# Performance work log

Hardware: AMD Instinct MI355X
Metric: run time of the kernel (lower is better)

Reference implementation:

```python
import jax, jax.numpy as jnp
import numpy as np
import math

B, S, H, NH = 2, 2048, 2048, 16
HD = H // NH
LAYER_NUMBER = 5
NORM_FACTOR = math.sqrt(HD) * LAYER_NUMBER  # sqrt(head_dim) * coeff
BETA = 1.0 / LAYER_NUMBER
SCALE = float(LAYER_NUMBER)  # ScaledSoftmax scale = coeff
MASK_VALUE = -10000.0


def setup_inputs() -> dict:
    key = jax.random.key(0)
    ks = jax.random.split(key, 6)
    inv_sqrt_h = 1.0 / math.sqrt(H)
    return {
        "hidden_states": jax.random.normal(ks[0], (B, S, H), jnp.float32),
        "alibi": jax.random.normal(ks[1], (NH, 1, S), jnp.float32) * 0.1,
        "w_qkv": jax.random.normal(ks[2], (3 * H, H), jnp.float32) * inv_sqrt_h,
        "b_qkv": jax.random.normal(ks[3], (3 * H,), jnp.float32) * 0.02,
        "w_dense": jax.random.normal(ks[4], (H, H), jnp.float32) * inv_sqrt_h,
        "b_dense": jax.random.normal(ks[5], (H,), jnp.float32) * 0.02,
        "attention_mask": jnp.ones((B, S), jnp.int32),
    }


def reference(hidden_states, alibi, w_qkv, b_qkv, w_dense, b_dense, attention_mask):
    b, s, h = hidden_states.shape
    # QKV projection: [b, s, 3h] -> [b, s, nh, 3*hd] -> split
    mixed = hidden_states @ w_qkv.T + b_qkv
    mixed = mixed.reshape(b, s, NH, 3 * HD)
    q, k, v = jnp.split(mixed, 3, axis=-1)  # each [b, s, nh, hd]

    # Faithful Megatron-style memory reinterpretation (row-major reshape),
    # exactly matching torch's .contiguous().view(s, b*nh, hd).
    q2 = jnp.swapaxes(q.reshape(s, b * NH, HD), 0, 1)  # [b*nh, q_len, hd]
    k2 = jnp.swapaxes(k.reshape(s, b * NH, HD), 0, 1)  # [b*nh, k_len, hd]
    v2 = jnp.swapaxes(v.reshape(s, b * NH, HD), 0, 1)  # [b*nh, k_len, hd]

    # baddbmm: alibi*beta + (q @ k^T)/norm_factor
    alibi_b = jnp.tile(alibi, (b, 1, 1))[: b * NH, :, :s]  # [b*nh, 1, k_len]
    scores = alibi_b * BETA + jnp.einsum("bqd,bkd->bqk", q2, k2) * (1.0 / NORM_FACTOR)
    scores = scores.reshape(b, NH, s, s)

    # ScaledSoftmax: scale then fused causal+padding mask fill, then softmax
    scores = scores * SCALE
    pad_bool = (1 - attention_mask).astype(bool)  # True where padded
    causal = jnp.tril(jnp.ones((s, s), dtype=bool))
    bad = pad_bool[:, None, :, None] | (~causal)[None, None, :, :]  # [b,1,s,s]
    scores = jnp.where(bad, MASK_VALUE, scores)
    probs = jax.nn.softmax(scores, axis=-1)  # [b, nh, s, s]

    # context = probs @ V with the same faithful reshapes
    probs_r = probs.reshape(b * NH, s, s)
    context = jnp.einsum("bqk,bkd->bqd", probs_r, v2)  # [b*nh, q_len, hd]
    context = context.reshape(b, NH, s, HD)
    context = jnp.transpose(context, (2, 0, 1, 3)).reshape(s, b, h)  # [s, b, h]

    out = context @ w_dense.T + b_dense  # [s, b, h]
    return jnp.swapaxes(out, 0, 1)  # [b, s, h]
```

## Files before the change

kernel.cpp:

```cpp
#include <hip/hip_runtime.h>

typedef unsigned short u16;
typedef __bf16  bf16x8 __attribute__((ext_vector_type(8)));
typedef float   f32x4  __attribute__((ext_vector_type(4)));
typedef u16     u16x8  __attribute__((ext_vector_type(8)));
typedef u16     u16x4  __attribute__((ext_vector_type(4)));

#define QSCALE 0.12751744545f

__device__ __forceinline__ u16 f2b(float f) {
    unsigned u = __float_as_uint(f);
    unsigned r = u + 0x7FFFu + ((u >> 16) & 1u);
    return (u16)(r >> 16);
}
__device__ __forceinline__ float b2f(u16 b) {
    return __uint_as_float(((unsigned)b) << 16);
}
__device__ __forceinline__ void async16(const u16* g, u16* l) {
    __builtin_amdgcn_global_load_lds(
        (__attribute__((address_space(1))) void*)(u16*)g,
        (__attribute__((address_space(3))) void*)l, 16, 0, 0);
}

__global__ void cvt_f32_bf16(const float* __restrict__ in, u16* __restrict__ out, int n4) {
    int i = blockIdx.x * blockDim.x + threadIdx.x;
    if (i >= n4) return;
    float4 f = ((const float4*)in)[i];
    u16x4 o;
    o[0] = f2b(f.x); o[1] = f2b(f.y); o[2] = f2b(f.z); o[3] = f2b(f.w);
    *(u16x4*)(out + (size_t)i * 4) = o;
}

__global__ void cvt_wqkv(const float* __restrict__ in, u16* __restrict__ out, int n4) {
    int i = blockIdx.x * blockDim.x + threadIdx.x;
    if (i >= n4) return;
    int row = i >> 9;
    float s = ((row % 384) < 128) ? QSCALE : 1.0f;
    float4 f = ((const float4*)in)[i];
    u16x4 o;
    o[0] = f2b(f.x * s); o[1] = f2b(f.y * s); o[2] = f2b(f.z * s); o[3] = f2b(f.w * s);
    *(u16x4*)(out + (size_t)i * 4) = o;
}

__global__ __launch_bounds__(256) void gemm_bt(
    const u16* __restrict__ A, const u16* __restrict__ B,
    const float* __restrict__ bias, void* __restrict__ C,
    u16* __restrict__ qb, u16* __restrict__ kb, u16* __restrict__ vb,
    int M, int N, int K, int mode)
{
    __shared__ u16 smem[16384];
    u16* As = smem;
    u16* Bs = smem + 8192;

    int tid = threadIdx.x, wave = tid >> 6, lane = tid & 63;
    int lg = lane >> 4, lm = lane & 15;
    int wm = (wave & 1) * 64, wn = (wave >> 1) * 64;

    const u16* Ab = A + (size_t)(blockIdx.y * 128) * K;
    const u16* Bb = B + (size_t)(blockIdx.x * 128) * K;

    f32x4 acc[4][4];
    for (int i = 0; i < 4; i++)
        for (int j = 0; j < 4; j++)
            acc[i][j] = (f32x4){0.f, 0.f, 0.f, 0.f};

    int srow = (lane >> 2), skq = (lane & 3) * 8;

    for (int k0 = 0; k0 < K; k0 += 64) {
        __syncthreads();
        for (int cc = wave; cc < 16; cc += 4) {
            int p = cc >> 3, c = cc & 7;
            int row = c * 16 + srow;
            size_t off = (size_t)row * K + k0 + p * 32 + skq;
            async16(Ab + off, &As[p * 4096 + c * 512]);
            async16(Bb + off, &Bs[p * 4096 + c * 512]);
        }
        __syncthreads();

        for (int p = 0; p < 2; p++) {
            bf16x8 af[4], bf[4];
            for (int i = 0; i < 4; i++) af[i] = *(const bf16x8*)&As[p * 4096 + (wm + i * 16 + lm) * 32 + lg * 8];
            for (int j = 0; j < 4; j++) bf[j] = *(const bf16x8*)&Bs[p * 4096 + (wn + j * 16 + lm) * 32 + lg * 8];
            for (int i = 0; i < 4; i++)
                for (int j = 0; j < 4; j++)
                    acc[i][j] = __builtin_amdgcn_mfma_f32_16x16x32_bf16(af[i], bf[j], acc[i][j], 0, 0, 0);
        }
    }

    if (mode == 1) {
        for (int j = 0; j < 4; j++) {
            int col = blockIdx.x * 128 + wn + j * 16 + lm;
            float bv = bias[col];
            for (int i = 0; i < 4; i++) {
                int row0 = blockIdx.y * 128 + wm + i * 16 + lg * 4;
                for (int r = 0; r < 4; r++) {
                    int row = row0 + r;
                    int orow = ((row & 1) << 11) + (row >> 1);
                    ((float*)C)[(size_t)orow * N + col] = acc[i][j][r] + bv;
                }
            }
        }
        return;
    }

    int ct = blockIdx.x;
    int nh = ct / 3, part = ct - nh * 3;
    float bscale = (part == 0) ? QSCALE : 1.0f;
    int rbase = blockIdx.y * 128;
    int b = rbase >> 11;
    int s0 = rbase & 2047;

    if (part < 2) {
        u16* dst0 = part ? kb : qb;
        for (int j = 0; j < 4; j++) {
            int hd = wn + j * 16 + lm;
            float bv = bias[ct * 128 + hd] * bscale;
            for (int i = 0; i < 4; i++) {
                for (int r = 0; r < 4; r++) {
                    int rl = wm + i * 16 + lg * 4 + r;
                    int s = s0 + rl;
                    int bn = (s & 1) * 16 + nh;
                    int pos = (b << 10) + (s >> 1);
                    dst0[((size_t)(bn * 2048 + pos)) * 128 + hd] = f2b(acc[i][j][r] + bv);
                }
            }
        }
    } else {
        u16 (*arr)[64][128] = (u16(*)[64][128])smem;
        __syncthreads();
        for (int j = 0; j < 4; j++) {
            int hd = wn + j * 16 + lm;
            float bv = bias[ct * 128 + hd];
            for (int i = 0; i < 4; i++) {
                for (int r = 0; r < 4; r++) {
                    int rl = wm + i * 16 + lg * 4 + r;
                    arr[rl & 1][rl >> 1][hd] = f2b(acc[i][j][r] + bv);
                }
            }
        }
        __syncthreads();
        int hd = tid & 127, par = tid >> 7;
        int bn = par * 16 + nh;
        int pos0 = (b << 10) + (s0 >> 1);
        u16* dst = vb + ((size_t)(bn * 128 + hd)) * 2048 + pos0;
        for (int c = 0; c < 8; c++) {
            u16x8 w;
            for (int e = 0; e < 8; e++) w[e] = arr[par][c * 8 + e][hd];
            *(u16x8*)(dst + c * 8) = w;
        }
    }
}

__global__ __launch_bounds__(256) void attn(
    const u16* __restrict__ qb, const u16* __restrict__ kb,
    const u16* __restrict__ vb, const float* __restrict__ alibi,
    u16* __restrict__ ctx)
{
    __shared__ u16 Ks[64 * 136];
    __shared__ u16 Vt[128 * 88];
    __shared__ u16 Ps[4][16 * 72];

    int bn = blockIdx.y;
    int tid = threadIdx.x, wave = tid >> 6, lane = tid & 63;
    int lg = lane >> 4, lm = lane & 15;

    const float* al = alibi + (bn & 15) * 2048;

    int krow = tid >> 2, kq = (tid & 3) * 32;
    int vhd  = tid >> 1, vh2 = (tid & 1) * 32;
    const u16* ksrc0 = kb + (size_t)(bn * 2048 + krow) * 128 + kq;
    const u16* vsrc0 = vb + (size_t)(bn * 128 + vhd) * 2048 + vh2;

    u16* ps = &Ps[wave][0];
    bf16x8 ones;
    {
        u16x8 t;
        for (int j = 0; j < 8; j++) t[j] = 0x3F80;
        ones = *(bf16x8*)&t;
    }

    for (int pass = 0; pass < 2; pass++) {
        int qt = pass ? (31 - blockIdx.x) : blockIdx.x;
        int q0 = qt * 64;

        bf16x8 qf[4];
        {
            const u16* qp = qb + ((size_t)bn * 2048 + q0 + wave * 16 + lm) * 128 + lg * 8;
            for (int kc = 0; kc < 4; kc++) qf[kc] = *(const bf16x8*)(qp + kc * 32);
        }

        f32x4 o[9];
        for (int i = 0; i < 9; i++) o[i] = (f32x4){0.f, 0.f, 0.f, 0.f};

        u16x8 kreg[4], vreg[4];
        for (int i = 0; i < 4; i++) kreg[i] = *(const u16x8*)(ksrc0 + i * 8);
        for (int i = 0; i < 4; i++) vreg[i] = *(const u16x8*)(vsrc0 + i * 8);

        for (int kt = 0; kt <= qt; kt++) {
            int k0 = kt * 64;
            __syncthreads();
            {
                u16* d1 = &Ks[krow * 136 + kq];
                for (int i = 0; i < 4; i++) *(u16x8*)(d1 + i * 8) = kreg[i];
                u16* d2 = &Vt[vhd * 88 + vh2];
                for (int i = 0; i < 4; i++) *(u16x8*)(d2 + i * 8) = vreg[i];
            }
            __syncthreads();

            if (kt < qt) {
                const u16* s1 = ksrc0 + (size_t)(kt + 1) * 64 * 128;
                const u16* s2 = vsrc0 + (kt + 1) * 64;
                for (int i = 0; i < 4; i++) kreg[i] = *(const u16x8*)(s1 + i * 8);
                for (int i = 0; i < 4; i++) vreg[i] = *(const u16x8*)(s2 + i * 8);
            }

            f32x4 sc[4];
            for (int tc = 0; tc < 4; tc++) {
                const u16* kr = &Ks[(tc * 16 + lm) * 136 + lg * 8];
                f32x4 a = (f32x4){0.f, 0.f, 0.f, 0.f};
                for (int kc = 0; kc < 4; kc++)
                    a = __builtin_amdgcn_mfma_f32_16x16x32_bf16(qf[kc], *(const bf16x8*)(kr + kc * 32), a, 0, 0, 0);
                sc[tc] = a;
            }

            bool diag = (kt == qt);
            for (int tc = 0; tc < 4; tc++) {
                int kg = k0 + tc * 16 + lm;
                float av = (al[kg] - 8.0f) * 1.4426950408889634f;
                for (int r = 0; r < 4; r++) {
                    float v = sc[tc][r] + av;
                    if (diag && kg > q0 + wave * 16 + lg * 4 + r) v = -3e38f;
                    ps[(lg * 4 + r) * 72 + tc * 16 + lm] = f2b(__builtin_amdgcn_exp2f(v));
                }
            }

            for (int kc = 0; kc < 2; kc++) {
                bf16x8 pf = *(const bf16x8*)&ps[lm * 72 + kc * 32 + lg * 8];
                for (int i = 0; i < 8; i++) {
                    bf16x8 vf = *(const bf16x8*)&Vt[(i * 16 + lm) * 88 + kc * 32 + lg * 8];
                    o[i] = __builtin_amdgcn_mfma_f32_16x16x32_bf16(pf, vf, o[i], 0, 0, 0);
                }
                o[8] = __builtin_amdgcn_mfma_f32_16x16x32_bf16(pf, ones, o[8], 0, 0, 0);
            }
        }

        for (int r = 0; r < 4; r++) {
            float inv = 1.0f / o[8][r];
            int qg = q0 + wave * 16 + lg * 4 + r;
            int row = qg * 2 + (bn >> 4);
            u16* crow = ctx + (size_t)row * 2048 + (bn & 15) * 128 + lm;
            for (int i = 0; i < 8; i++)
                crow[i * 16] = f2b(o[i][r] * inv);
        }
    }
}

extern "C" void kernel_launch(void* const* d_in, const int* in_sizes, int n_in,
                              void* d_out, int out_size, void* d_ws, size_t ws_size,
                              hipStream_t stream)
{
    const float* hs    = (const float*)d_in[0];
    const float* alibi = (const float*)d_in[1];
    const float* wqkv  = (const float*)d_in[2];
    const float* bqkv  = (const float*)d_in[3];
    const float* wd    = (const float*)d_in[4];
    const float* bd    = (const float*)d_in[5];
    float* out = (float*)d_out;

    char* ws = (char*)d_ws;
    u16* wqkv_b = (u16*)(ws + 0);
    u16* hs_b   = (u16*)(ws + 25165824);
    u16* ctx    = (u16*)(ws + 41943040);
    u16* wd_b   = wqkv_b;
    u16* qb     = (u16*)(ws + 92274688);
    u16* kb     = (u16*)(ws + 109051904);
    u16* vb     = (u16*)(ws + 125829120);

    cvt_f32_bf16<<<8192,  256, 0, stream>>>(hs,   hs_b,   2097152);
    cvt_wqkv   <<<12288, 256, 0, stream>>>(wqkv, wqkv_b, 3145728);

    gemm_bt<<<dim3(48, 32), 256, 0, stream>>>(hs_b, wqkv_b, bqkv, nullptr,
                                              qb, kb, vb, 4096, 6144, 2048, 0);

    cvt_f32_bf16<<<4096, 256, 0, stream>>>(wd, wd_b, 1048576);

    attn<<<dim3(16, 32), 256, 0, stream>>>(qb, kb, vb, alibi, ctx);

    gemm_bt<<<dim3(16, 32), 256, 0, stream>>>(ctx, wd_b, bd, out,
                                              nullptr, nullptr, nullptr, 4096, 2048, 2048, 1);
}
```

Before: 399.2 us.

## Use 32x32 MFMA with 128-row query tiles and double-buffered K/V in attention

Result: slower. 500.0 us (+25.3%).

```diff
diff --git a/kernel.cpp b/kernel.cpp
--- a/kernel.cpp
+++ b/kernel.cpp
@@ -3,6 +3,7 @@
 typedef unsigned short u16;
 typedef __bf16  bf16x8 __attribute__((ext_vector_type(8)));
 typedef float   f32x4  __attribute__((ext_vector_type(4)));
+typedef float   f32x16 __attribute__((ext_vector_type(16)));
 typedef u16     u16x8  __attribute__((ext_vector_type(8)));
 typedef u16     u16x4  __attribute__((ext_vector_type(4)));
 
@@ -151,18 +152,18 @@
     }
 }
 
-__global__ __launch_bounds__(256) void attn(
+__global__ __launch_bounds__(256, 1) void attn(
     const u16* __restrict__ qb, const u16* __restrict__ kb,
     const u16* __restrict__ vb, const float* __restrict__ alibi,
     u16* __restrict__ ctx)
 {
-    __shared__ u16 Ks[64 * 136];
-    __shared__ u16 Vt[128 * 88];
-    __shared__ u16 Ps[4][16 * 72];
+    __shared__ u16 Ks[2][64 * 140];
+    __shared__ u16 Vt[2][128 * 90];
+    __shared__ u16 Ps[4][32 * 74];
 
     int bn = blockIdx.y;
     int tid = threadIdx.x, wave = tid >> 6, lane = tid & 63;
-    int lg = lane >> 4, lm = lane & 15;
+    int ln = lane & 31, lh = lane >> 5;
 
     const float* al = alibi + (bn & 15) * 2048;
 
@@ -180,77 +181,85 @@
     }
 
     for (int pass = 0; pass < 2; pass++) {
-        int qt = pass ? (31 - blockIdx.x) : blockIdx.x;
-        int q0 = qt * 64;
-
-        bf16x8 qf[4];
+        int qt = pass ? (15 - blockIdx.x) : blockIdx.x;
+        int q0w = qt * 128 + wave * 32;
+        int ktmax = 2 * qt + 1;
+
+        bf16x8 qf[8];
         {
-            const u16* qp = qb + ((size_t)bn * 2048 + q0 + wave * 16 + lm) * 128 + lg * 8;
-            for (int kc = 0; kc < 4; kc++) qf[kc] = *(const bf16x8*)(qp + kc * 32);
-        }
-
-        f32x4 o[9];
-        for (int i = 0; i < 9; i++) o[i] = (f32x4){0.f, 0.f, 0.f, 0.f};
+            const u16* qp = qb + ((size_t)bn * 2048 + q0w + ln) * 128 + lh * 8;
+            for (int ks = 0; ks < 8; ks++) qf[ks] = *(const bf16x8*)(qp + ks * 16);
+        }
+
+        f32x16 o[4], sums;
+        for (int e = 0; e < 16; e++) { sums[e] = 0.f; o[0][e] = 0.f; o[1][e] = 0.f; o[2][e] = 0.f; o[3][e] = 0.f; }
 
         u16x8 kreg[4], vreg[4];
         for (int i = 0; i < 4; i++) kreg[i] = *(const u16x8*)(ksrc0 + i * 8);
         for (int i = 0; i < 4; i++) vreg[i] = *(const u16x8*)(vsrc0 + i * 8);
-
-        for (int kt = 0; kt <= qt; kt++) {
+        {
+            u16* d1 = &Ks[0][krow * 140 + kq];
+            for (int i = 0; i < 4; i++) *(u16x8*)(d1 + i * 8) = kreg[i];
+            u16* d2 = &Vt[0][vhd * 90 + vh2];
+            for (int i = 0; i < 4; i++) *(u16x8*)(d2 + i * 8) = vreg[i];
+        }
+        __syncthreads();
+
+        for (int kt = 0; kt <= ktmax; kt++) {
+            int cur = kt & 1;
             int k0 = kt * 64;
-            __syncthreads();
-            {
-                u16* d1 = &Ks[krow * 136 + kq];
-                for (int i = 0; i < 4; i++) *(u16x8*)(d1 + i * 8) = kreg[i];
-                u16* d2 = &Vt[vhd * 88 + vh2];
-                for (int i = 0; i < 4; i++) *(u16x8*)(d2 + i * 8) = vreg[i];
-            }
-            __syncthreads();
-
-            if (kt < qt) {
+
+            if (kt < ktmax) {
                 const u16* s1 = ksrc0 + (size_t)(kt + 1) * 64 * 128;
                 const u16* s2 = vsrc0 + (kt + 1) * 64;
                 for (int i = 0; i < 4; i++) kreg[i] = *(const u16x8*)(s1 + i * 8);
                 for (int i = 0; i < 4; i++) vreg[i] = *(const u16x8*)(s2 + i * 8);
             }
 
-            f32x4 sc[4];
-            for (int tc = 0; tc < 4; tc++) {
-                const u16* kr = &Ks[(tc * 16 + lm) * 136 + lg * 8];
-                f32x4 a = (f32x4){0.f, 0.f, 0.f, 0.f};
-                for (int kc = 0; kc < 4; kc++)
-                    a = __builtin_amdgcn_mfma_f32_16x16x32_bf16(qf[kc], *(const bf16x8*)(kr + kc * 32), a, 0, 0, 0);
-                sc[tc] = a;
-            }
-
-            bool diag = (kt == qt);
-            for (int tc = 0; tc < 4; tc++) {
-                int kg = k0 + tc * 16 + lm;
+            bool domask = (k0 + 63 > q0w);
+            for (int ct = 0; ct < 2; ct++) {
+                const u16* kr = &Ks[cur][(ct * 32 + ln) * 140 + lh * 8];
+                f32x16 a;
+                for (int e = 0; e < 16; e++) a[e] = 0.f;
+                for (int ks = 0; ks < 8; ks++)
+                    a = __builtin_amdgcn_mfma_f32_32x32x16_bf16(qf[ks], *(const bf16x8*)(kr + ks * 16), a, 0, 0, 0);
+
+                int kg = k0 + ct * 32 + ln;
                 float av = (al[kg] - 8.0f) * 1.4426950408889634f;
-                for (int r = 0; r < 4; r++) {
-                    float v = sc[tc][r] + av;
-                    if (diag && kg > q0 + wave * 16 + lg * 4 + r) v = -3e38f;
-                    ps[(lg * 4 + r) * 72 + tc * 16 + lm] = f2b(__builtin_amdgcn_exp2f(v));
-                }
-            }
-
-            for (int kc = 0; kc < 2; kc++) {
-                bf16x8 pf = *(const bf16x8*)&ps[lm * 72 + kc * 32 + lg * 8];
-                for (int i = 0; i < 8; i++) {
-                    bf16x8 vf = *(const bf16x8*)&Vt[(i * 16 + lm) * 88 + kc * 32 + lg * 8];
-                    o[i] = __builtin_amdgcn_mfma_f32_16x16x32_bf16(pf, vf, o[i], 0, 0, 0);
-                }
-                o[8] = __builtin_amdgcn_mfma_f32_16x16x32_bf16(pf, ones, o[8], 0, 0, 0);
-            }
-        }
-
-        for (int r = 0; r < 4; r++) {
-            float inv = 1.0f / o[8][r];
-            int qg = q0 + wave * 16 + lg * 4 + r;
-            int row = qg * 2 + (bn >> 4);
-            u16* crow = ctx + (size_t)row * 2048 + (bn & 15) * 128 + lm;
-            for (int i = 0; i < 8; i++)
-                crow[i * 16] = f2b(o[i][r] * inv);
+                for (int reg = 0; reg < 16; reg++) {
+                    int row = (reg & 3) + 8 * (reg >> 2) + 4 * lh;
+                    float v = a[reg] + av;
+                    if (domask && kg > q0w + row) v = -3e38f;
+                    ps[row * 74 + ct * 32 + ln] = f2b(__builtin_amdgcn_exp2f(v));
+                }
+            }
+
+            for (int ks = 0; ks < 4; ks++) {
+                bf16x8 pa = *(const bf16x8*)&ps[ln * 74 + ks * 16 + lh * 8];
+                sums = __builtin_amdgcn_mfma_f32_32x32x16_bf16(pa, ones, sums, 0, 0, 0);
+                for (int ht = 0; ht < 4; ht++) {
+                    bf16x8 vf = *(const bf16x8*)&Vt[cur][(ht * 32 + ln) * 90 + ks * 16 + lh * 8];
+                    o[ht] = __builtin_amdgcn_mfma_f32_32x32x16_bf16(pa, vf, o[ht], 0, 0, 0);
+                }
+            }
+
+            if (kt < ktmax) {
+                u16* d1 = &Ks[cur ^ 1][krow * 140 + kq];
+                for (int i = 0; i < 4; i++) *(u16x8*)(d1 + i * 8) = kreg[i];
+                u16* d2 = &Vt[cur ^ 1][vhd * 90 + vh2];
+                for (int i = 0; i < 4; i++) *(u16x8*)(d2 + i * 8) = vreg[i];
+            }
+            __syncthreads();
+        }
+
+        for (int reg = 0; reg < 16; reg++) {
+            int row = (reg & 3) + 8 * (reg >> 2) + 4 * lh;
+            float inv = 1.0f / sums[reg];
+            int qg = q0w + row;
+            int crow = qg * 2 + (bn >> 4);
+            u16* cp = ctx + (size_t)crow * 2048 + (bn & 15) * 128 + ln;
+            for (int ht = 0; ht < 4; ht++)
+                cp[ht * 32] = f2b(o[ht][reg] * inv);
         }
     }
 }
@@ -284,7 +293,7 @@
 
     cvt_f32_bf16<<<4096, 256, 0, stream>>>(wd, wd_b, 1048576);
 
-    attn<<<dim3(16, 32), 256, 0, stream>>>(qb, kb, vb, alibi, ctx);
+    attn<<<dim3(8, 32), 256, 0, stream>>>(qb, kb, vb, alibi, ctx);
 
     gemm_bt<<<dim3(16, 32), 256, 0, stream>>>(ctx, wd_b, bd, out,
                                               nullptr, nullptr, nullptr, 4096, 2048, 2048, 1);
```

## Split causal attention KV range across two blocks with fp32 partials and finalize kernel

Applied to the files above, without the earlier changes.

Measured after the change: 463.8 us. 16.2% more time.

```diff
diff --git a/kernel.cpp b/kernel.cpp
--- a/kernel.cpp
+++ b/kernel.cpp
@@ -151,16 +151,16 @@
     }
 }
 
-__global__ __launch_bounds__(256) void attn(
+__global__ __launch_bounds__(256, 2) void attn(
     const u16* __restrict__ qb, const u16* __restrict__ kb,
     const u16* __restrict__ vb, const float* __restrict__ alibi,
-    u16* __restrict__ ctx)
+    float* __restrict__ Opart, float* __restrict__ Spart)
 {
-    __shared__ u16 Ks[64 * 136];
-    __shared__ u16 Vt[128 * 88];
-    __shared__ u16 Ps[4][16 * 72];
-
-    int bn = blockIdx.y;
+    __shared__ u16 Ks[64 * 140];
+    __shared__ u16 Vt[128 * 90];
+    __shared__ u16 Ps[4][32 * 76];
+
+    int j = blockIdx.x, bn = blockIdx.y;
     int tid = threadIdx.x, wave = tid >> 6, lane = tid & 63;
     int lg = lane >> 4, lm = lane & 15;
 
@@ -175,84 +175,136 @@
     bf16x8 ones;
     {
         u16x8 t;
-        for (int j = 0; j < 8; j++) t[j] = 0x3F80;
+        for (int e = 0; e < 8; e++) t[e] = 0x3F80;
         ones = *(bf16x8*)&t;
     }
 
-    for (int pass = 0; pass < 2; pass++) {
-        int qt = pass ? (31 - blockIdx.x) : blockIdx.x;
-        int q0 = qt * 64;
-
-        bf16x8 qf[4];
+    int part, qts[2], kA[2], kB[2];
+    if (j < 8) {
+        part = 0;
+        qts[0] = 15 - j; kA[0] = 0;      kB[0] = 15 - j;
+        qts[1] = j;      kA[1] = 0;      kB[1] = j;
+    } else {
+        part = 1;
+        qts[0] = j;      kA[0] = j + 1;  kB[0] = 2 * j + 1;
+        qts[1] = 15 - j; kA[1] = 16 - j; kB[1] = 31 - 2 * j;
+    }
+
+    for (int s = 0; s < 2; s++) {
+        int qt = qts[s], ktA = kA[s], ktB = kB[s];
+        int q0w = qt * 128 + wave * 32;
+
+        bf16x8 qf[2][4];
+        for (int i = 0; i < 2; i++) {
+            const u16* qp = qb + ((size_t)bn * 2048 + q0w + i * 16 + lm) * 128 + lg * 8;
+            for (int kc = 0; kc < 4; kc++) qf[i][kc] = *(const bf16x8*)(qp + kc * 32);
+        }
+
+        f32x4 o[2][8], sums[2];
+        for (int i = 0; i < 2; i++) {
+            sums[i] = (f32x4){0.f, 0.f, 0.f, 0.f};
+            for (int h = 0; h < 8; h++) o[i][h] = (f32x4){0.f, 0.f, 0.f, 0.f};
+        }
+
+        u16x8 kreg[4], vreg[4];
         {
-            const u16* qp = qb + ((size_t)bn * 2048 + q0 + wave * 16 + lm) * 128 + lg * 8;
-            for (int kc = 0; kc < 4; kc++) qf[kc] = *(const bf16x8*)(qp + kc * 32);
-        }
-
-        f32x4 o[9];
-        for (int i = 0; i < 9; i++) o[i] = (f32x4){0.f, 0.f, 0.f, 0.f};
-
-        u16x8 kreg[4], vreg[4];
-        for (int i = 0; i < 4; i++) kreg[i] = *(const u16x8*)(ksrc0 + i * 8);
-        for (int i = 0; i < 4; i++) vreg[i] = *(const u16x8*)(vsrc0 + i * 8);
-
-        for (int kt = 0; kt <= qt; kt++) {
+            const u16* s1 = ksrc0 + (size_t)ktA * 64 * 128;
+            const u16* s2 = vsrc0 + ktA * 64;
+            for (int i = 0; i < 4; i++) kreg[i] = *(const u16x8*)(s1 + i * 8);
+            for (int i = 0; i < 4; i++) vreg[i] = *(const u16x8*)(s2 + i * 8);
+        }
+
+        for (int kt = ktA; kt <= ktB; kt++) {
             int k0 = kt * 64;
             __syncthreads();
             {
-                u16* d1 = &Ks[krow * 136 + kq];
+                u16* d1 = &Ks[krow * 140 + kq];
                 for (int i = 0; i < 4; i++) *(u16x8*)(d1 + i * 8) = kreg[i];
-                u16* d2 = &Vt[vhd * 88 + vh2];
+                u16* d2 = &Vt[vhd * 90 + vh2];
                 for (int i = 0; i < 4; i++) *(u16x8*)(d2 + i * 8) = vreg[i];
             }
             __syncthreads();
 
-            if (kt < qt) {
+            if (kt < ktB) {
                 const u16* s1 = ksrc0 + (size_t)(kt + 1) * 64 * 128;
                 const u16* s2 = vsrc0 + (kt + 1) * 64;
                 for (int i = 0; i < 4; i++) kreg[i] = *(const u16x8*)(s1 + i * 8);
                 for (int i = 0; i < 4; i++) vreg[i] = *(const u16x8*)(s2 + i * 8);
             }
 
-            f32x4 sc[4];
+            bool domask = (k0 + 63 > q0w);
             for (int tc = 0; tc < 4; tc++) {
-                const u16* kr = &Ks[(tc * 16 + lm) * 136 + lg * 8];
-                f32x4 a = (f32x4){0.f, 0.f, 0.f, 0.f};
-                for (int kc = 0; kc < 4; kc++)
-                    a = __builtin_amdgcn_mfma_f32_16x16x32_bf16(qf[kc], *(const bf16x8*)(kr + kc * 32), a, 0, 0, 0);
-                sc[tc] = a;
-            }
-
-            bool diag = (kt == qt);
-            for (int tc = 0; tc < 4; tc++) {
+                const u16* kr = &Ks[(tc * 16 + lm) * 140 + lg * 8];
+                f32x4 a0 = (f32x4){0.f, 0.f, 0.f, 0.f};
+                f32x4 a1 = (f32x4){0.f, 0.f, 0.f, 0.f};
+                for (int kc = 0; kc < 4; kc++) {
+                    bf16x8 bfr = *(const bf16x8*)(kr + kc * 32);
+                    a0 = __builtin_amdgcn_mfma_f32_16x16x32_bf16(qf[0][kc], bfr, a0, 0, 0, 0);
+                    a1 = __builtin_amdgcn_mfma_f32_16x16x32_bf16(qf[1][kc], bfr, a1, 0, 0, 0);
+                }
                 int kg = k0 + tc * 16 + lm;
                 float av = (al[kg] - 8.0f) * 1.4426950408889634f;
                 for (int r = 0; r < 4; r++) {
-                    float v = sc[tc][r] + av;
-                    if (diag && kg > q0 + wave * 16 + lg * 4 + r) v = -3e38f;
-                    ps[(lg * 4 + r) * 72 + tc * 16 + lm] = f2b(__builtin_amdgcn_exp2f(v));
+                    float v0 = a0[r] + av, v1 = a1[r] + av;
+                    if (domask) {
+                        int r0 = q0w + lg * 4 + r;
+                        if (kg > r0) v0 = -3e38f;
+                        if (kg > r0 + 16) v1 = -3e38f;
+                    }
+                    ps[(lg * 4 + r) * 76 + tc * 16 + lm]        = f2b(__builtin_amdgcn_exp2f(v0));
+                    ps[(16 + lg * 4 + r) * 76 + tc * 16 + lm]   = f2b(__builtin_amdgcn_exp2f(v1));
                 }
             }
 
             for (int kc = 0; kc < 2; kc++) {
-                bf16x8 pf = *(const bf16x8*)&ps[lm * 72 + kc * 32 + lg * 8];
-                for (int i = 0; i < 8; i++) {
-                    bf16x8 vf = *(const bf16x8*)&Vt[(i * 16 + lm) * 88 + kc * 32 + lg * 8];
-                    o[i] = __builtin_amdgcn_mfma_f32_16x16x32_bf16(pf, vf, o[i], 0, 0, 0);
-                }
-                o[8] = __builtin_amdgcn_mfma_f32_16x16x32_bf16(pf, ones, o[8], 0, 0, 0);
-            }
-        }
-
-        for (int r = 0; r < 4; r++) {
-            float inv = 1.0f / o[8][r];
-            int qg = q0 + wave * 16 + lg * 4 + r;
-            int row = qg * 2 + (bn >> 4);
-            u16* crow = ctx + (size_t)row * 2048 + (bn & 15) * 128 + lm;
-            for (int i = 0; i < 8; i++)
-                crow[i * 16] = f2b(o[i][r] * inv);
-        }
-    }
+                bf16x8 pf0 = *(const bf16x8*)&ps[lm * 76 + kc * 32 + lg * 8];
+                bf16x8 pf1 = *(const bf16x8*)&ps[(16 + lm) * 76 + kc * 32 + lg * 8];
+                for (int ht = 0; ht < 8; ht++) {
+                    bf16x8 vf = *(const bf16x8*)&Vt[(ht * 16 + lm) * 90 + kc * 32 + lg * 8];
+                    o[0][ht] = __builtin_amdgcn_mfma_f32_16x16x32_bf16(pf0, vf, o[0][ht], 0, 0, 0);
+                    o[1][ht] = __builtin_amdgcn_mfma_f32_16x16x32_bf16(pf1, vf, o[1][ht], 0, 0, 0);
+                }
+                sums[0] = __builtin_amdgcn_mfma_f32_16x16x32_bf16(pf0, ones, sums[0], 0, 0, 0);
+                sums[1] = __builtin_amdgcn_mfma_f32_16x16x32_bf16(pf1, ones, sums[1], 0, 0, 0);
+            }
+        }
+
+        float* Op = Opart + (((size_t)part * 32 + bn) * 2048 + qt * 128) * 128;
+        for (int i = 0; i < 2; i++)
+            for (int r = 0; r < 4; r++) {
+                int row = wave * 32 + i * 16 + lg * 4 + r;
+                float* orow = Op + (size_t)row * 128 + lm;
+                for (int ht = 0; ht < 8; ht++) orow[ht * 16] = o[i][ht][r];
+            }
+        if (lm == 0) {
+            float* Sp = Spart + ((size_t)part * 32 + bn) * 2048 + qt * 128 + wave * 32;
+            for (int i = 0; i < 2; i++)
+                for (int r = 0; r < 4; r++)
+                    Sp[i * 16 + lg * 4 + r] = sums[i][r];
+        }
+    }
+}
+
+__global__ void attn_fin(const float* __restrict__ Opart, const float* __restrict__ Spart,
+                         u16* __restrict__ ctx)
+{
+    int idx = blockIdx.x * 256 + threadIdx.x;
+    int hd8 = idx & 15;
+    int q   = (idx >> 4) & 2047;
+    int bn  = idx >> 15;
+    size_t o0 = (((size_t)bn) * 2048 + q) * 128 + hd8 * 8;
+    size_t o1 = (size_t)32 * 2048 * 128 + o0;
+    float s = Spart[bn * 2048 + q] + Spart[32 * 2048 + bn * 2048 + q];
+    float inv = 1.0f / s;
+    const float4* A = (const float4*)(Opart + o0);
+    const float4* B = (const float4*)(Opart + o1);
+    float4 a0 = A[0], a1 = A[1], b0 = B[0], b1 = B[1];
+    u16x8 w;
+    w[0] = f2b((a0.x + b0.x) * inv); w[1] = f2b((a0.y + b0.y) * inv);
+    w[2] = f2b((a0.z + b0.z) * inv); w[3] = f2b((a0.w + b0.w) * inv);
+    w[4] = f2b((a1.x + b1.x) * inv); w[5] = f2b((a1.y + b1.y) * inv);
+    w[6] = f2b((a1.z + b1.z) * inv); w[7] = f2b((a1.w + b1.w) * inv);
+    *(u16x8*)(ctx + ((size_t)(q * 2 + (bn >> 4))) * 2048 + (bn & 15) * 128 + hd8 * 8) = w;
 }
 
 extern "C" void kernel_launch(void* const* d_in, const int* in_sizes, int n_in,
@@ -268,13 +320,15 @@
     float* out = (float*)d_out;
 
     char* ws = (char*)d_ws;
-    u16* wqkv_b = (u16*)(ws + 0);
-    u16* hs_b   = (u16*)(ws + 25165824);
-    u16* ctx    = (u16*)(ws + 41943040);
-    u16* wd_b   = wqkv_b;
-    u16* qb     = (u16*)(ws + 92274688);
-    u16* kb     = (u16*)(ws + 109051904);
-    u16* vb     = (u16*)(ws + 125829120);
+    u16*   wqkv_b = (u16*)(ws + 0);
+    u16*   hs_b   = (u16*)(ws + 25165824);
+    float* Opart  = (float*)(ws + 0);
+    u16*   ctx    = (u16*)(ws + 67108864);
+    u16*   wd_b   = (u16*)(ws + 83886080);
+    u16*   qb     = (u16*)(ws + 92274688);
+    u16*   kb     = (u16*)(ws + 109051904);
+    u16*   vb     = (u16*)(ws + 125829120);
+    float* Spart  = (float*)d_out;
 
     cvt_f32_bf16<<<8192,  256, 0, stream>>>(hs,   hs_b,   2097152);
     cvt_wqkv   <<<12288, 256, 0, stream>>>(wqkv, wqkv_b, 3145728);
@@ -284,7 +338,8 @@
 
     cvt_f32_bf16<<<4096, 256, 0, stream>>>(wd, wd_b, 1048576);
 
-    attn<<<dim3(16, 32), 256, 0, stream>>>(qb, kb, vb, alibi, ctx);
+    attn<<<dim3(16, 32), 256, 0, stream>>>(qb, kb, vb, alibi, Opart, Spart);
+    attn_fin<<<4096, 256, 0, stream>>>(Opart, Spart, ctx);
 
     gemm_bt<<<dim3(16, 32), 256, 0, stream>>>(ctx, wd_b, bd, out,
                                               nullptr, nullptr, nullptr, 4096, 2048, 2048, 1);
```
